# Optimization experiments

Measured on AMD Instinct MI355X. Metric: run time of the kernel, lower is better.

The kernel has to match this reference:

```python
import jax, jax.numpy as jnp
import numpy as np

N, L, D, H, HIST = 4, 1024, 1024, 16, 128
HD = D // H          # head_dim = 64
SCALE = D ** 0.5     # note: original scales by sqrt(model_dim), not sqrt(head_dim)


def _band_mask():
    # get_mask: tril XOR tril(diag=-history_len) -> True inside the causal band.
    # masked_fill fills where mask is True, so pass the complement (True outside band).
    r = jnp.arange(L)[:, None]
    c = jnp.arange(L)[None, :]
    band = (c <= r) & (c > r - HIST)  # band of width HIST incl. diagonal
    return jnp.broadcast_to(~band, (N, 1, L, L))


def setup_inputs() -> dict:
    key = jax.random.key(0)
    ks = jax.random.split(key, 8)
    s = 0.02
    return {
        "values": jax.random.normal(ks[0], (N, L, D), jnp.float32),
        "keys": jax.random.normal(ks[1], (N, L, D), jnp.float32),
        "query": jax.random.normal(ks[2], (N, L, D), jnp.float32),
        "mask": _band_mask(),
        "Wv": jax.random.normal(ks[3], (HD, HD), jnp.float32) * s,
        "Wk": jax.random.normal(ks[4], (HD, HD), jnp.float32) * s,
        "Wq": jax.random.normal(ks[5], (HD, HD), jnp.float32) * s,
        "Wo": jax.random.normal(ks[6], (D, D), jnp.float32) * s,
        "bo": jax.random.normal(ks[7], (D,), jnp.float32) * s,
    }


def reference(values, keys, query, mask, Wv, Wk, Wq, Wo, bo):
    n, qlen, _ = query.shape
    # split heads and apply per-head linear projections (nn.Linear: x @ W.T)
    v = values.reshape(n, -1, H, HD) @ Wv.T
    k = keys.reshape(n, -1, H, HD) @ Wk.T
    q = query.reshape(n, qlen, H, HD) @ Wq.T
    # full energy [n, h, q, k]
    energy = jnp.einsum('nqhd,nkhd->nhqk', q, k)
    energy = jnp.where(mask, jnp.float32(-1e20), energy)
    scores = jax.nn.softmax(energy / SCALE, axis=-1)
    # NOTE: faithful to original einsum 'nhql,nlhd->nlhd' (reduces over q):
    # attention[n,l,h,d] = (sum_q scores[n,h,q,l]) * v[n,l,h,d]
    attention = jnp.einsum('nhql,nlhd->nlhd', scores, v)
    out = attention.reshape(n, qlen, D) @ Wo.T + bo
    return out
```

## Files before the change

kernel.cpp:

```cpp
#include <hip/hip_runtime.h>
#include <hip/hip_bf16.h>
#include <math.h>


using short8 = __attribute__((ext_vector_type(8))) short;
using f32x4  = __attribute__((ext_vector_type(4))) float;

__device__ __forceinline__ unsigned short f2bf(float x) {
    unsigned u = __float_as_uint(x);
    u += 0x7FFFu + ((u >> 16) & 1u);
    return (unsigned short)(u >> 16);
}

__global__ __launch_bounds__(256) void kM2(const float* __restrict__ Wq,
                                           const float* __restrict__ Wk,
                                           const float* __restrict__ Wv,
                                           float* __restrict__ M,
                                           unsigned short* __restrict__ Wvb) {
    int idx = blockIdx.x * 256 + threadIdx.x;
    int e = idx >> 6, f = idx & 63;
    float s = 0.f;
#pragma unroll 8
    for (int d = 0; d < 64; ++d) s = fmaf(Wq[d * 64 + e], Wk[d * 64 + f], s);
    M[idx] = s * (1.0f / 32.0f);
    Wvb[idx] = f2bf(Wv[idx]);
}

__global__ __launch_bounds__(256) void k_cw(const float4* __restrict__ Wo4,
                                            ushort4* __restrict__ Wob4) {
    int idx = blockIdx.x * 256 + threadIdx.x;
    float4 v = Wo4[idx];
    ushort4 o;
    o.x = f2bf(v.x); o.y = f2bf(v.y); o.z = f2bf(v.z); o.w = f2bf(v.w);
    Wob4[idx] = o;
}

__global__ __launch_bounds__(256) void k_kb(const float* __restrict__ keys,
                                            unsigned short* __restrict__ kbp) {
    const int tid  = threadIdx.x;
    const int b    = blockIdx.x;
    const int tile = b & 15;
    const int nh   = b >> 4;
    const int h    = nh & 15;
    const int n    = nh >> 4;
    const int t0   = tile * 64;

    const float* kbase = keys + ((size_t)(n * 1024 + t0)) * 1024 + h * 64;
    unsigned short* kout = kbp + ((size_t)(nh * 1024 + t0)) * 64;
#pragma unroll
    for (int i = 0; i < 4; ++i) {
        int idx = tid + i * 256;
        int r = idx >> 4, f0 = (idx & 15) * 4;
        float4 kv = *reinterpret_cast<const float4*>(kbase + (size_t)r * 1024 + f0);
        ushort4 ko; ko.x = f2bf(kv.x); ko.y = f2bf(kv.y);
        ko.z = f2bf(kv.z); ko.w = f2bf(kv.w);
        *reinterpret_cast<ushort4*>(kout + (size_t)r * 64 + f0) = ko;
    }
}

__global__ __launch_bounds__(256) void k_w2f(const float* __restrict__ query,
                                             const unsigned short* __restrict__ kbp,
                                             const float* __restrict__ Mm,
                                             float* __restrict__ w) {
    __shared__ unsigned short xqA[64 * 72];
    __shared__ unsigned short Mt[64 * 72];
    __shared__ unsigned short yqA[64 * 72];
    __shared__ float wloc[192];

    const int tid  = threadIdx.x;
    const int b    = blockIdx.x;
    const int tile = b & 15;
    const int nh   = b >> 4;
    const int h    = nh & 15;
    const int n    = nh >> 4;
    const int t0   = tile * 64;

    if (tid < 192) wloc[tid] = 0.f;

    for (int idx = tid; idx < 4096; idx += 256) {
        int e = idx >> 6, f = idx & 63;
        Mt[f * 72 + e] = f2bf(Mm[idx]);
    }
    {
        const float* qbase = query + ((size_t)(n * 1024 + t0)) * 1024 + h * 64;
#pragma unroll
        for (int i = 0; i < 4; ++i) {
            int idx = tid + i * 256;
            int r = idx >> 4, f0 = (idx & 15) * 4;
            float4 qv = *reinterpret_cast<const float4*>(qbase + (size_t)r * 1024 + f0);
            ushort4 qo; qo.x = f2bf(qv.x); qo.y = f2bf(qv.y);
            qo.z = f2bf(qv.z); qo.w = f2bf(qv.w);
            *reinterpret_cast<ushort4*>(&xqA[r * 72 + f0]) = qo;
        }
    }
    __syncthreads();

    const int wv = tid >> 6, lane = tid & 63;
    const int m = lane & 15, q4 = lane >> 4, ksel = q4 * 8;

    {
        short8 af[2];
#pragma unroll
        for (int ch = 0; ch < 2; ++ch)
            af[ch] = *reinterpret_cast<const short8*>(
                &xqA[(wv * 16 + m) * 72 + ch * 32 + ksel]);
        f32x4 acc[4];
#pragma unroll
        for (int fc = 0; fc < 4; ++fc) {
            acc[fc] = f32x4{0.f, 0.f, 0.f, 0.f};
#pragma unroll
            for (int ch = 0; ch < 2; ++ch) {
                short8 bf = *reinterpret_cast<const short8*>(
                    &Mt[(fc * 16 + m) * 72 + ch * 32 + ksel]);
                acc[fc] = __builtin_amdgcn_mfma_f32_16x16x32_bf16(af[ch], bf, acc[fc], 0, 0, 0);
            }
        }
#pragma unroll
        for (int fc = 0; fc < 4; ++fc)
#pragma unroll
            for (int r = 0; r < 4; ++r)
                yqA[(wv * 16 + q4 * 4 + r) * 72 + fc * 16 + m] = f2bf(acc[fc][r]);
    }
    __syncthreads();

    const unsigned short* ya = &yqA[(wv * 16 + m) * 72];
    short8 af0 = *reinterpret_cast<const short8*>(ya + ksel);
    short8 af1 = *reinterpret_cast<const short8*>(ya + 32 + ksel);

    const unsigned short* kb = kbp + (size_t)nh * 1024 * 64;
    short8 bfr[12][2];
#pragma unroll
    for (int ni = 0; ni < 12; ++ni) {
        int l = t0 - 127 + ni * 16 + m;
        int lc = min(max(l, 0), 1023);
        const unsigned short* kp = kb + (size_t)lc * 64 + ksel;
        bfr[ni][0] = *reinterpret_cast<const short8*>(kp);
        bfr[ni][1] = *reinterpret_cast<const short8*>(kp + 32);
    }

    f32x4 acc[12];
#pragma unroll
    for (int ni = 0; ni < 12; ++ni) {
        acc[ni] = f32x4{0.f, 0.f, 0.f, 0.f};
        acc[ni] = __builtin_amdgcn_mfma_f32_16x16x32_bf16(af0, bfr[ni][0], acc[ni], 0, 0, 0);
        acc[ni] = __builtin_amdgcn_mfma_f32_16x16x32_bf16(af1, bfr[ni][1], acc[ni], 0, 0, 0);
    }

    const int rbase = wv * 16 + q4 * 4;
    float rs[4] = {0.f, 0.f, 0.f, 0.f};
#pragma unroll
    for (int ni = 0; ni < 12; ++ni) {
        const int c = ni * 16 + m;
#pragma unroll
        for (int reg = 0; reg < 4; ++reg) {
            const int rlw = rbase + reg;
            bool valid = (c >= rlw) && (c <= rlw + 127) && (c + t0 >= 127);
            float e = valid ? __expf(acc[ni][reg]) : 0.f;
            acc[ni][reg] = e;
            rs[reg] += e;
        }
    }
#pragma unroll
    for (int reg = 0; reg < 4; ++reg) {
#pragma unroll
        for (int mm = 1; mm < 16; mm <<= 1) rs[reg] += __shfl_xor(rs[reg], mm);
        rs[reg] = 1.0f / rs[reg];
    }
#pragma unroll
    for (int ni = 0; ni < 12; ++ni) {
        float cs = acc[ni][0] * rs[0] + acc[ni][1] * rs[1] +
                   acc[ni][2] * rs[2] + acc[ni][3] * rs[3];
        cs += __shfl_xor(cs, 16);
        cs += __shfl_xor(cs, 32);
        if (lane < 16) atomicAdd(&wloc[ni * 16 + m], cs);
    }
    __syncthreads();

    for (int c = tid; c < 192; c += 256) {
        int l = t0 - 127 + c;
        if (l >= 0 && l < 1024)
            atomicAdd(&w[(size_t)nh * 1024 + l], wloc[c]);
    }
}

__global__ __launch_bounds__(256) void k_ap2(const float* __restrict__ values,
                                             const unsigned short* __restrict__ Wvb,
                                             const float* __restrict__ w,
                                             unsigned short* __restrict__ apb) {
    const int tid = threadIdx.x;
    const long R0 = (long)blockIdx.x * 64;
    const int wv = tid >> 6, lane = tid & 63;
    const int m = lane & 15, ksel = (lane >> 4) * 8;

    const float* va = values + (R0 + wv * 16 + m) * 64;
    short8 af[2];
#pragma unroll
    for (int ch = 0; ch < 2; ++ch) {
        float4 x0 = *reinterpret_cast<const float4*>(va + ch * 32 + ksel);
        float4 x1 = *reinterpret_cast<const float4*>(va + ch * 32 + ksel + 4);
        short8 a;
        a[0] = (short)f2bf(x0.x); a[1] = (short)f2bf(x0.y);
        a[2] = (short)f2bf(x0.z); a[3] = (short)f2bf(x0.w);
        a[4] = (short)f2bf(x1.x); a[5] = (short)f2bf(x1.y);
        a[6] = (short)f2bf(x1.z); a[7] = (short)f2bf(x1.w);
        af[ch] = a;
    }

    f32x4 acc[4];
#pragma unroll
    for (int dc = 0; dc < 4; ++dc) {
        acc[dc] = f32x4{0.f, 0.f, 0.f, 0.f};
#pragma unroll
        for (int ch = 0; ch < 2; ++ch) {
            short8 bf = *reinterpret_cast<const short8*>(
                Wvb + (size_t)(dc * 16 + m) * 64 + ch * 32 + ksel);
            acc[dc] = __builtin_amdgcn_mfma_f32_16x16x32_bf16(af[ch], bf, acc[dc], 0, 0, 0);
        }
    }

    const long rowb = R0 + wv * 16 + (lane >> 4) * 4;
    float wf[4];
#pragma unroll
    for (int reg = 0; reg < 4; ++reg) {
        long rg = rowb + reg;
        int hh = (int)(rg & 15);
        int ll = (int)((rg >> 4) & 1023);
        int nn = (int)(rg >> 14);
        wf[reg] = w[((size_t)(nn * 16 + hh) << 10) + ll];
    }
#pragma unroll
    for (int dc = 0; dc < 4; ++dc)
#pragma unroll
        for (int reg = 0; reg < 4; ++reg)
            apb[(size_t)(rowb + reg) * 64 + dc * 16 + m] = f2bf(acc[dc][reg] * wf[reg]);
}

__global__ __launch_bounds__(256) void k_out_mfma(
    const unsigned short* __restrict__ apb,
    const unsigned short* __restrict__ wob,
    const float* __restrict__ bo,
    float* __restrict__ out) {
    __shared__ unsigned short As[128 * 32];
    __shared__ unsigned short Bs[128 * 32];

    const int tid  = threadIdx.x;
    const int wv   = tid >> 6;
    const int lane = tid & 63;
    const int wy   = wv >> 1, wx = wv & 1;

    const int bx = blockIdx.x & 7;
    const int by = blockIdx.x >> 3;
    const long arow0 = (long)by * 128;
    const int  bcol0 = bx * 128;

    f32x4 acc[4][4];
#pragma unroll
    for (int mi = 0; mi < 4; ++mi)
#pragma unroll
        for (int ni = 0; ni < 4; ++ni) acc[mi][ni] = f32x4{0.f, 0.f, 0.f, 0.f};

    const int r0s = tid >> 2;
    const int kks = (tid & 3) * 8;

    for (int kt = 0; kt < 32; ++kt) {
        const int k0 = kt * 32;
#pragma unroll
        for (int i = 0; i < 2; ++i) {
            const unsigned short* g =
                apb + (arow0 + i * 64 + r0s) * 1024 + k0 + kks;
            __builtin_amdgcn_global_load_lds(
                (const __attribute__((address_space(1))) unsigned int*)g,
                (__attribute__((address_space(3))) unsigned int*)&As[i * 2048 + wv * 512],
                16, 0, 0);
        }
#pragma unroll
        for (int i = 0; i < 2; ++i) {
            const unsigned short* g =
                wob + (size_t)(bcol0 + i * 64 + r0s) * 1024 + k0 + kks;
            __builtin_amdgcn_global_load_lds(
                (const __attribute__((address_space(1))) unsigned int*)g,
                (__attribute__((address_space(3))) unsigned int*)&Bs[i * 2048 + wv * 512],
                16, 0, 0);
        }
        __syncthreads();

        const int koff = (lane >> 4) * 8;
        const int rA = wy * 64 + (lane & 15);
        const int rB = wx * 64 + (lane & 15);
        short8 af[4], bf[4];
#pragma unroll
        for (int mi = 0; mi < 4; ++mi)
            af[mi] = *reinterpret_cast<const short8*>(&As[(rA + mi * 16) * 32 + koff]);
#pragma unroll
        for (int ni = 0; ni < 4; ++ni)
            bf[ni] = *reinterpret_cast<const short8*>(&Bs[(rB + ni * 16) * 32 + koff]);
#pragma unroll
        for (int mi = 0; mi < 4; ++mi)
#pragma unroll
            for (int ni = 0; ni < 4; ++ni)
                acc[mi][ni] = __builtin_amdgcn_mfma_f32_16x16x32_bf16(
                    af[mi], bf[ni], acc[mi][ni], 0, 0, 0);
        __syncthreads();
    }

    const int colb = bcol0 + wx * 64 + (lane & 15);
    const int rowb = (int)arow0 + wy * 64 + (lane >> 4) * 4;
#pragma unroll
    for (int ni = 0; ni < 4; ++ni) {
        const int col = colb + ni * 16;
        const float bias = bo[col];
#pragma unroll
        for (int mi = 0; mi < 4; ++mi) {
            const int row = rowb + mi * 16;
#pragma unroll
            for (int r = 0; r < 4; ++r)
                out[(size_t)(row + r) * 1024 + col] = acc[mi][ni][r] + bias;
        }
    }
}

extern "C" void kernel_launch(void* const* d_in, const int* in_sizes, int n_in,
                              void* d_out, int out_size, void* d_ws, size_t ws_size,
                              hipStream_t stream) {
    const float* values = (const float*)d_in[0];
    const float* keys   = (const float*)d_in[1];
    const float* query  = (const float*)d_in[2];
    const float* Wv     = (const float*)d_in[4];
    const float* Wk     = (const float*)d_in[5];
    const float* Wq     = (const float*)d_in[6];
    const float* Wo     = (const float*)d_in[7];
    const float* bo     = (const float*)d_in[8];
    float* out = (float*)d_out;

    float* Mws = (float*)d_ws;
    float* w   = Mws + 4096;
    unsigned short* Wvb = (unsigned short*)(w + 65536);
    unsigned short* wob = Wvb + 4096;
    unsigned short* kbp = wob + 1024 * 1024;
    unsigned short* apb = kbp;

    hipMemsetAsync(w, 0, 65536 * sizeof(float), stream);
    kM2<<<16, 256, 0, stream>>>(Wq, Wk, Wv, Mws, Wvb);
    k_cw<<<1024, 256, 0, stream>>>((const float4*)Wo, (ushort4*)wob);
    k_kb<<<1024, 256, 0, stream>>>(keys, kbp);
    k_w2f<<<1024, 256, 0, stream>>>(query, kbp, Mws, w);
    k_ap2<<<1024, 256, 0, stream>>>(values, Wvb, w, apb);
    k_out_mfma<<<256, 256, 0, stream>>>(apb, wob, bo, out);
}
```

Before: 169.7 us.

## Merge prep kernels and memset into one launch, load query fragments directly

Folds the weight products, Wo and key bf16 conversions, and the zeroing of w into a single prep kernel, replacing a memset and three launches with one. The prep kernel now writes the M matrix pre-transposed in bf16, so the scores kernel reads MFMA B fragments straight from global memory. Query A fragments are likewise loaded and converted directly into registers, dropping two shared-memory tiles and one barrier. The apb buffer gets its own region instead of aliasing kbp. Costs are uncoalesced per-lane global reads for M and query fragments, and the M computation now runs concurrently with the key conversion instead of before it.

```diff
diff --git a/kernel.cpp b/kernel.cpp
--- a/kernel.cpp
+++ b/kernel.cpp
@@ -12,31 +12,56 @@
     return (unsigned short)(u >> 16);
 }
 
-__global__ __launch_bounds__(256) void kM2(const float* __restrict__ Wq,
-                                           const float* __restrict__ Wk,
-                                           const float* __restrict__ Wv,
-                                           float* __restrict__ M,
-                                           unsigned short* __restrict__ Wvb) {
-    int idx = blockIdx.x * 256 + threadIdx.x;
-    int e = idx >> 6, f = idx & 63;
-    float s = 0.f;
+__global__ __launch_bounds__(256) void k_prep(const float* __restrict__ keys,
+                                              const float* __restrict__ Wq,
+                                              const float* __restrict__ Wk,
+                                              const float* __restrict__ Wv,
+                                              const float4* __restrict__ Wo4,
+                                              unsigned short* __restrict__ kbp,
+                                              float* __restrict__ w,
+                                              ushort4* __restrict__ wob4,
+                                              unsigned short* __restrict__ Mtb,
+                                              unsigned short* __restrict__ Wvb) {
+    const int b = blockIdx.x, tid = threadIdx.x;
+    if (b < 1024) {
+        const int tile = b & 15, nh = b >> 4, h = nh & 15, n = nh >> 4;
+        const int t0 = tile * 64;
+        const float* kbase = keys + ((size_t)(n * 1024 + t0)) * 1024 + h * 64;
+        unsigned short* kout = kbp + ((size_t)(nh * 1024 + t0)) * 64;
+#pragma unroll
+        for (int i = 0; i < 4; ++i) {
+            int idx = tid + i * 256;
+            int r = idx >> 4, f0 = (idx & 15) * 4;
+            float4 kv = *reinterpret_cast<const float4*>(kbase + (size_t)r * 1024 + f0);
+            ushort4 ko; ko.x = f2bf(kv.x); ko.y = f2bf(kv.y);
+            ko.z = f2bf(kv.z); ko.w = f2bf(kv.w);
+            *reinterpret_cast<ushort4*>(kout + (size_t)r * 64 + f0) = ko;
+        }
+        if (tid < 64) w[b * 64 + tid] = 0.f;
+    } else if (b < 2048) {
+        int idx = (b - 1024) * 256 + tid;
+        float4 v = Wo4[idx];
+        ushort4 o; o.x = f2bf(v.x); o.y = f2bf(v.y);
+        o.z = f2bf(v.z); o.w = f2bf(v.w);
+        wob4[idx] = o;
+    } else {
+        int idx = (b - 2048) * 256 + tid;
+        int e = idx >> 6, f = idx & 63;
+        float s = 0.f;
 #pragma unroll 8
-    for (int d = 0; d < 64; ++d) s = fmaf(Wq[d * 64 + e], Wk[d * 64 + f], s);
-    M[idx] = s * (1.0f / 32.0f);
-    Wvb[idx] = f2bf(Wv[idx]);
-}
-
-__global__ __launch_bounds__(256) void k_cw(const float4* __restrict__ Wo4,
-                                            ushort4* __restrict__ Wob4) {
-    int idx = blockIdx.x * 256 + threadIdx.x;
-    float4 v = Wo4[idx];
-    ushort4 o;
-    o.x = f2bf(v.x); o.y = f2bf(v.y); o.z = f2bf(v.z); o.w = f2bf(v.w);
-    Wob4[idx] = o;
-}
-
-__global__ __launch_bounds__(256) void k_kb(const float* __restrict__ keys,
-                                            unsigned short* __restrict__ kbp) {
+        for (int d = 0; d < 64; ++d) s = fmaf(Wq[d * 64 + e], Wk[d * 64 + f], s);
+        Mtb[f * 64 + e] = f2bf(s * (1.0f / 32.0f));
+        Wvb[idx] = f2bf(Wv[idx]);
+    }
+}
+
+__global__ __launch_bounds__(256) void k_w2(const float* __restrict__ query,
+                                            const unsigned short* __restrict__ kbp,
+                                            const unsigned short* __restrict__ Mtb,
+                                            float* __restrict__ w) {
+    __shared__ unsigned short yqA[64 * 72];
+    __shared__ float wloc[192];
+
     const int tid  = threadIdx.x;
     const int b    = blockIdx.x;
     const int tile = b & 15;
@@ -45,65 +70,25 @@
     const int n    = nh >> 4;
     const int t0   = tile * 64;
 
-    const float* kbase = keys + ((size_t)(n * 1024 + t0)) * 1024 + h * 64;
-    unsigned short* kout = kbp + ((size_t)(nh * 1024 + t0)) * 64;
-#pragma unroll
-    for (int i = 0; i < 4; ++i) {
-        int idx = tid + i * 256;
-        int r = idx >> 4, f0 = (idx & 15) * 4;
-        float4 kv = *reinterpret_cast<const float4*>(kbase + (size_t)r * 1024 + f0);
-        ushort4 ko; ko.x = f2bf(kv.x); ko.y = f2bf(kv.y);
-        ko.z = f2bf(kv.z); ko.w = f2bf(kv.w);
-        *reinterpret_cast<ushort4*>(kout + (size_t)r * 64 + f0) = ko;
-    }
-}
-
-__global__ __launch_bounds__(256) void k_w2f(const float* __restrict__ query,
-                                             const unsigned short* __restrict__ kbp,
-                                             const float* __restrict__ Mm,
-                                             float* __restrict__ w) {
-    __shared__ unsigned short xqA[64 * 72];
-    __shared__ unsigned short Mt[64 * 72];
-    __shared__ unsigned short yqA[64 * 72];
-    __shared__ float wloc[192];
-
-    const int tid  = threadIdx.x;
-    const int b    = blockIdx.x;
-    const int tile = b & 15;
-    const int nh   = b >> 4;
-    const int h    = nh & 15;
-    const int n    = nh >> 4;
-    const int t0   = tile * 64;
-
     if (tid < 192) wloc[tid] = 0.f;
-
-    for (int idx = tid; idx < 4096; idx += 256) {
-        int e = idx >> 6, f = idx & 63;
-        Mt[f * 72 + e] = f2bf(Mm[idx]);
-    }
-    {
-        const float* qbase = query + ((size_t)(n * 1024 + t0)) * 1024 + h * 64;
-#pragma unroll
-        for (int i = 0; i < 4; ++i) {
-            int idx = tid + i * 256;
-            int r = idx >> 4, f0 = (idx & 15) * 4;
-            float4 qv = *reinterpret_cast<const float4*>(qbase + (size_t)r * 1024 + f0);
-            ushort4 qo; qo.x = f2bf(qv.x); qo.y = f2bf(qv.y);
-            qo.z = f2bf(qv.z); qo.w = f2bf(qv.w);
-            *reinterpret_cast<ushort4*>(&xqA[r * 72 + f0]) = qo;
-        }
-    }
-    __syncthreads();
 
     const int wv = tid >> 6, lane = tid & 63;
     const int m = lane & 15, q4 = lane >> 4, ksel = q4 * 8;
 
     {
+        const float* qrow = query + ((size_t)(n * 1024 + t0 + wv * 16 + m)) * 1024 + h * 64;
         short8 af[2];
 #pragma unroll
-        for (int ch = 0; ch < 2; ++ch)
-            af[ch] = *reinterpret_cast<const short8*>(
-                &xqA[(wv * 16 + m) * 72 + ch * 32 + ksel]);
+        for (int ch = 0; ch < 2; ++ch) {
+            float4 x0 = *reinterpret_cast<const float4*>(qrow + ch * 32 + ksel);
+            float4 x1 = *reinterpret_cast<const float4*>(qrow + ch * 32 + ksel + 4);
+            short8 a;
+            a[0] = (short)f2bf(x0.x); a[1] = (short)f2bf(x0.y);
+            a[2] = (short)f2bf(x0.z); a[3] = (short)f2bf(x0.w);
+            a[4] = (short)f2bf(x1.x); a[5] = (short)f2bf(x1.y);
+            a[6] = (short)f2bf(x1.z); a[7] = (short)f2bf(x1.w);
+            af[ch] = a;
+        }
         f32x4 acc[4];
 #pragma unroll
         for (int fc = 0; fc < 4; ++fc) {
@@ -111,7 +96,7 @@
 #pragma unroll
             for (int ch = 0; ch < 2; ++ch) {
                 short8 bf = *reinterpret_cast<const short8*>(
-                    &Mt[(fc * 16 + m) * 72 + ch * 32 + ksel]);
+                    Mtb + (size_t)(fc * 16 + m) * 64 + ch * 32 + ksel);
                 acc[fc] = __builtin_amdgcn_mfma_f32_16x16x32_bf16(af[ch], bf, acc[fc], 0, 0, 0);
             }
         }
@@ -332,18 +317,16 @@
     const float* bo     = (const float*)d_in[8];
     float* out = (float*)d_out;
 
-    float* Mws = (float*)d_ws;
-    float* w   = Mws + 4096;
-    unsigned short* Wvb = (unsigned short*)(w + 65536);
+    float* w            = (float*)d_ws;
+    unsigned short* Mtb = (unsigned short*)(w + 65536);
+    unsigned short* Wvb = Mtb + 4096;
     unsigned short* wob = Wvb + 4096;
     unsigned short* kbp = wob + 1024 * 1024;
-    unsigned short* apb = kbp;
-
-    hipMemsetAsync(w, 0, 65536 * sizeof(float), stream);
-    kM2<<<16, 256, 0, stream>>>(Wq, Wk, Wv, Mws, Wvb);
-    k_cw<<<1024, 256, 0, stream>>>((const float4*)Wo, (ushort4*)wob);
-    k_kb<<<1024, 256, 0, stream>>>(keys, kbp);
-    k_w2f<<<1024, 256, 0, stream>>>(query, kbp, Mws, w);
+    unsigned short* apb = kbp + 64 * 1024 * 64;
+
+    k_prep<<<2064, 256, 0, stream>>>(keys, Wq, Wk, Wv, (const float4*)Wo,
+                                     kbp, w, (ushort4*)wob, Mtb, Wvb);
+    k_w2<<<1024, 256, 0, stream>>>(query, kbp, Mtb, w);
     k_ap2<<<1024, 256, 0, stream>>>(values, Wvb, w, apb);
     k_out_mfma<<<256, 256, 0, stream>>>(apb, wob, bo, out);
 }
```

Result: faster. 166.2 us (-2.0%).
